# Kernel tuning notes

Hardware: AMD Instinct MI355X
Metric: run time of the kernel (lower is better)

The kernel has to match this reference:

```python
import jax, jax.numpy as jnp
import numpy as np

B, T, D, H, L = 1024, 512, 16, 30, 10


def setup_inputs() -> dict:
    key = jax.random.key(0)
    ks = jax.random.split(key, 8)
    s = 1.0 / np.sqrt(H)  # PyTorch RNN init scale (uniform +-1/sqrt(H)); normal*s is fine for a numeric baseline
    return {
        "x": jax.random.normal(ks[0], (B, T, D), dtype=jnp.float32),
        "W_ih0": jax.random.normal(ks[1], (H, D), dtype=jnp.float32) * s,
        "W_ih": jax.random.normal(ks[2], (L - 1, H, H), dtype=jnp.float32) * s,
        "W_hh": jax.random.normal(ks[3], (L, H, H), dtype=jnp.float32) * s,
        "b_ih": jax.random.normal(ks[4], (L, H), dtype=jnp.float32) * s,
        "b_hh": jax.random.normal(ks[5], (L, H), dtype=jnp.float32) * s,
        "fc_w": jax.random.normal(ks[6], (1, H), dtype=jnp.float32) * s,
        "fc_b": jax.random.normal(ks[7], (1,), dtype=jnp.float32) * s,
    }


def _rnn_layer(x, Wi, Wh, bi, bh):
    # x: [B, T, Din] -> [B, T, H]; h_t = tanh(x_t Wi^T + bi + h_{t-1} Wh^T + bh)
    xw = jnp.einsum("btd,hd->bth", x, Wi) + (bi + bh)  # fold both biases once
    h0 = jnp.zeros((x.shape[0], Wh.shape[0]), dtype=x.dtype)

    def step(h, xw_t):
        h = jnp.tanh(xw_t + h @ Wh.T)
        return h, h

    _, ys = jax.lax.scan(step, h0, jnp.swapaxes(xw, 0, 1))  # scan over time
    return jnp.swapaxes(ys, 0, 1)


def reference(x, W_ih0, W_ih, W_hh, b_ih, b_hh, fc_w, fc_b):
    out = _rnn_layer(x, W_ih0, W_hh[0], b_ih[0], b_hh[0])
    for l in range(1, L):
        out = _rnn_layer(out, W_ih[l - 1], W_hh[l], b_ih[l], b_hh[l])
    # fc on last timestep: [B, H] @ [H, 1] + b -> [B, 1]
    return out[:, -1, :] @ fc_w.T + fc_b
```

## Files before the change

kernel.cpp:

```cpp
#include <hip/hip_runtime.h>

#define TT 512
#define DD 16
#define HH 30
#define LL 10
#define C  4
#define TCH (TT / C)
#define RING 4
#define GRP 16
#define BLOCKT (LL * 64)
#define KPRE 2.885390081777927f

#define CC_H   512
#define SL_H   (C * CC_H)
#define LINK_H (RING * SL_H)

typedef _Float16 f16x8 __attribute__((ext_vector_type(8)));
typedef _Float16 h2    __attribute__((ext_vector_type(2)));
typedef float    f32x4 __attribute__((ext_vector_type(4)));

union U128 { uint4 u; f16x8 h; h2 p[4]; };

__device__ __forceinline__ float sigma_e(float d) {
    const float e = __builtin_amdgcn_exp2f(d);
    return __builtin_amdgcn_rcpf(e + 1.0f);
}

__device__ __forceinline__ int nu_of(int k) {
    return 16 * ((k >> 2) & 1) + 4 * (k >> 3) + (k & 3);
}

__device__ __forceinline__ void wait_ge(unsigned* f, unsigned tgt) {
    while (__hip_atomic_load(f, __ATOMIC_ACQUIRE,
                             __HIP_MEMORY_SCOPE_WORKGROUP) < tgt)
        __builtin_amdgcn_s_sleep(1);
}

__global__ __launch_bounds__(BLOCKT) void rnn_sig(
    const float* __restrict__ x,   const float* __restrict__ wi0,
    const float* __restrict__ wih, const float* __restrict__ whh,
    const float* __restrict__ bih, const float* __restrict__ bhh,
    const float* __restrict__ fcw, const float* __restrict__ fcb,
    float* __restrict__ out)
{
    extern __shared__ __align__(16) _Float16 link[];
    __shared__ unsigned flg[2 * LL];

    const int tid  = threadIdx.x;
    const int l    = tid >> 6;
    const int lane = tid & 63;
    const int n    = lane & 15;
    const int qq   = lane >> 4;
    const int b0   = blockIdx.x * GRP;

    f16x8 wain[2], waown[2];
    #pragma unroll
    for (int tile = 0; tile < 2; ++tile) {
        const int j = 16 * tile + n;
        #pragma unroll
        for (int i = 0; i < 8; ++i) {
            const int kap = 8 * qq + i;
            const int nu  = nu_of(kap);
            float vi = 0.f, vo = 0.f;
            if (j < HH) {
                if (l == 0) { if (kap < DD) vi =  wi0[j * DD + kap]; }
                else        { if (nu  < HH) vi = -2.f * wih[(l - 1) * 900 + j * HH + nu]; }
                if (nu < HH) vo = -2.f * whh[l * 900 + j * HH + nu];
            }
            wain[tile][i]  = (_Float16)(vi * KPRE);
            waown[tile][i] = (_Float16)(vo * KPRE);
        }
    }
    f32x4 cb[2];
    #pragma unroll
    for (int tile = 0; tile < 2; ++tile)
        #pragma unroll
        for (int r = 0; r < 4; ++r) {
            const int j2 = 16 * tile + 4 * qq + r;
            float v = 0.f;
            if (j2 < HH) {
                v = bih[l * HH + j2] + bhh[l * HH + j2];
                for (int k = 0; k < HH; ++k) v += whh[l * 900 + j2 * HH + k];
                if (l > 0)
                    for (int k = 0; k < HH; ++k) v += wih[(l - 1) * 900 + j2 * HH + k];
            }
            cb[tile][r] = v * KPRE;
        }
    float fcl[8];
    #pragma unroll
    for (int i = 0; i < 8; ++i) {
        const int nu = nu_of(8 * qq + i);
        fcl[i] = (nu < HH) ? -2.f * fcw[nu] : 0.f;
    }
    float fbv = fcb[0];
    for (int k = 0; k < HH; ++k) fbv += fcw[k];

    float4 xb[C][2];
    const float4* x4 = (const float4*)x;
    const size_t xbase = (size_t)(b0 + n) * TT * 4;
    if (l == 0 && qq < 2) {
        #pragma unroll
        for (int cc = 0; cc < C; ++cc) {
            xb[cc][0] = x4[xbase + cc * 4 + 2 * qq];
            xb[cc][1] = x4[xbase + cc * 4 + 2 * qq + 1];
        }
    }

    _Float16* lin_r = link + (l - 1) * LINK_H + lane * 8;
    _Float16* lin_w = link + l * LINK_H + lane * 8;

    f16x8 bown;
    #pragma unroll
    for (int i = 0; i < 8; ++i) bown[i] = (_Float16)0.5f;

    if (tid < 2 * LL) flg[tid] = 0u;
    __syncthreads();

    for (int pb = 0; pb < TCH; pb += RING) {
        #pragma unroll
        for (int sl = 0; sl < RING; ++sl) {
            const int pt = pb + sl;

            U128 binu[C];
            if (l == 0) {
                #pragma unroll
                for (int cc = 0; cc < C; ++cc) {
                    if (qq < 2) {
                        const float4 u = xb[cc][0], v = xb[cc][1];
                        binu[cc].p[0] = (h2)__builtin_amdgcn_cvt_pkrtz(u.x, u.y);
                        binu[cc].p[1] = (h2)__builtin_amdgcn_cvt_pkrtz(u.z, u.w);
                        binu[cc].p[2] = (h2)__builtin_amdgcn_cvt_pkrtz(v.x, v.y);
                        binu[cc].p[3] = (h2)__builtin_amdgcn_cvt_pkrtz(v.z, v.w);
                        if (pt + 1 < TCH) {
                            const int tn = (pt + 1) * C + cc;
                            xb[cc][0] = x4[xbase + tn * 4 + 2 * qq];
                            xb[cc][1] = x4[xbase + tn * 4 + 2 * qq + 1];
                        }
                    } else {
                        binu[cc].u = uint4{0u, 0u, 0u, 0u};
                    }
                }
            } else {
                wait_ge(&flg[l - 1], (unsigned)(pt + 1));
                #pragma unroll
                for (int cc = 0; cc < C; ++cc)
                    binu[cc].u = *(const uint4*)(lin_r + sl * SL_H + cc * CC_H);
            }

            f32x4 dp0[C], dp1[C];
            #pragma unroll
            for (int cc = 0; cc < C; ++cc) {
                dp0[cc] = __builtin_amdgcn_mfma_f32_16x16x32_f16(wain[0], binu[cc].h, cb[0], 0, 0, 0);
                dp1[cc] = __builtin_amdgcn_mfma_f32_16x16x32_f16(wain[1], binu[cc].h, cb[1], 0, 0, 0);
            }
            if (l > 0 && lane == 0)
                __hip_atomic_store(&flg[LL + l], (unsigned)(pt + 1),
                                   __ATOMIC_RELEASE, __HIP_MEMORY_SCOPE_WORKGROUP);
            if (l < LL - 1 && pt >= RING)
                wait_ge(&flg[LL + l + 1], (unsigned)(pt - RING + 1));

            #pragma unroll
            for (int cc = 0; cc < C; ++cc) {
                const f32x4 d0 = __builtin_amdgcn_mfma_f32_16x16x32_f16(waown[0], bown, dp0[cc], 0, 0, 0);
                const f32x4 d1 = __builtin_amdgcn_mfma_f32_16x16x32_f16(waown[1], bown, dp1[cc], 0, 0, 0);
                U128 uu;
                uu.p[0] = (h2)__builtin_amdgcn_cvt_pkrtz(sigma_e(d0[0]), sigma_e(d0[1]));
                uu.p[1] = (h2)__builtin_amdgcn_cvt_pkrtz(sigma_e(d0[2]), sigma_e(d0[3]));
                uu.p[2] = (h2)__builtin_amdgcn_cvt_pkrtz(sigma_e(d1[0]), sigma_e(d1[1]));
                uu.p[3] = (h2)__builtin_amdgcn_cvt_pkrtz(sigma_e(d1[2]), sigma_e(d1[3]));
                bown = uu.h;
                if (l < LL - 1)
                    *(uint4*)(lin_w + sl * SL_H + cc * CC_H) = uu.u;
            }
            if (l < LL - 1 && lane == 0)
                __hip_atomic_store(&flg[l], (unsigned)(pt + 1),
                                   __ATOMIC_RELEASE, __HIP_MEMORY_SCOPE_WORKGROUP);
        }
    }

    if (l == LL - 1) {
        float v = 0.f;
        #pragma unroll
        for (int i = 0; i < 8; ++i) v = fmaf((float)bown[i], fcl[i], v);
        v += __shfl_xor(v, 16);
        v += __shfl_xor(v, 32);
        if (qq == 0) out[b0 + n] = v + fbv;
    }
}

extern "C" void kernel_launch(void* const* d_in, const int* in_sizes, int n_in,
                              void* d_out, int out_size, void* d_ws, size_t ws_size,
                              hipStream_t stream) {
    const float* x   = (const float*)d_in[0];
    const float* wi0 = (const float*)d_in[1];
    const float* wih = (const float*)d_in[2];
    const float* whh = (const float*)d_in[3];
    const float* bih = (const float*)d_in[4];
    const float* bhh = (const float*)d_in[5];
    const float* fcw = (const float*)d_in[6];
    const float* fcb = (const float*)d_in[7];
    float* out = (float*)d_out;

    const size_t lds_bytes = (size_t)(LL - 1) * LINK_H * sizeof(_Float16);
    hipFuncSetAttribute((const void*)rnn_sig,
                        hipFuncAttributeMaxDynamicSharedMemorySize,
                        (int)lds_bytes);

    rnn_sig<<<1024 / GRP, BLOCKT, lds_bytes, stream>>>(x, wi0, wih, whh,
                                                       bih, bhh, fcw, fcb, out);
}
```

Baseline: 204.4 us.

## Double-buffer layer inputs and prefetch next slot before recurrent MFMA

Each layer wavefront now loads the next time slot's input from the LDS link (or converts prefetched x for layer 0) into a second register buffer while the current step's recurrent MFMAs and sigmoids run. This hides LDS read and flag-wait latency behind compute. The downstream back-pressure wait moves from every step to once per ring block, and the spin-wait drops s_sleep for lower wake latency. In exchange it uses more registers, and busy-polling with no sleep adds LDS traffic.

```diff
diff --git a/kernel.cpp b/kernel.cpp
--- a/kernel.cpp
+++ b/kernel.cpp
@@ -32,11 +32,10 @@
 
 __device__ __forceinline__ void wait_ge(unsigned* f, unsigned tgt) {
     while (__hip_atomic_load(f, __ATOMIC_ACQUIRE,
-                             __HIP_MEMORY_SCOPE_WORKGROUP) < tgt)
-        __builtin_amdgcn_s_sleep(1);
-}
-
-__global__ __launch_bounds__(BLOCKT) void rnn_sig(
+                             __HIP_MEMORY_SCOPE_WORKGROUP) < tgt) {}
+}
+
+__global__ __launch_bounds__(BLOCKT) void rnn_pipe(
     const float* __restrict__ x,   const float* __restrict__ wi0,
     const float* __restrict__ wih, const float* __restrict__ whh,
     const float* __restrict__ bih, const float* __restrict__ bhh,
@@ -95,69 +94,92 @@
     float fbv = fcb[0];
     for (int k = 0; k < HH; ++k) fbv += fcw[k];
 
+    _Float16* lin_r = link + (l - 1) * LINK_H + lane * 8;
+    _Float16* lin_w = link + l * LINK_H + lane * 8;
+
+    f16x8 bown;
+    #pragma unroll
+    for (int i = 0; i < 8; ++i) bown[i] = (_Float16)0.5f;
+
+    if (tid < 2 * LL) flg[tid] = 0u;
+    __syncthreads();
+
+    U128 bin[2][C];
     float4 xb[C][2];
     const float4* x4 = (const float4*)x;
     const size_t xbase = (size_t)(b0 + n) * TT * 4;
-    if (l == 0 && qq < 2) {
+
+    if (l == 0) {
         #pragma unroll
         for (int cc = 0; cc < C; ++cc) {
-            xb[cc][0] = x4[xbase + cc * 4 + 2 * qq];
-            xb[cc][1] = x4[xbase + cc * 4 + 2 * qq + 1];
-        }
-    }
-
-    _Float16* lin_r = link + (l - 1) * LINK_H + lane * 8;
-    _Float16* lin_w = link + l * LINK_H + lane * 8;
-
-    f16x8 bown;
-    #pragma unroll
-    for (int i = 0; i < 8; ++i) bown[i] = (_Float16)0.5f;
-
-    if (tid < 2 * LL) flg[tid] = 0u;
-    __syncthreads();
+            bin[0][cc].u = uint4{0u, 0u, 0u, 0u};
+            bin[1][cc].u = uint4{0u, 0u, 0u, 0u};
+        }
+        if (qq < 2) {
+            #pragma unroll
+            for (int cc = 0; cc < C; ++cc) {
+                const float4 u = x4[xbase + cc * 4 + 2 * qq];
+                const float4 v = x4[xbase + cc * 4 + 2 * qq + 1];
+                bin[0][cc].p[0] = (h2)__builtin_amdgcn_cvt_pkrtz(u.x, u.y);
+                bin[0][cc].p[1] = (h2)__builtin_amdgcn_cvt_pkrtz(u.z, u.w);
+                bin[0][cc].p[2] = (h2)__builtin_amdgcn_cvt_pkrtz(v.x, v.y);
+                bin[0][cc].p[3] = (h2)__builtin_amdgcn_cvt_pkrtz(v.z, v.w);
+                xb[cc][0] = x4[xbase + (C + cc) * 4 + 2 * qq];
+                xb[cc][1] = x4[xbase + (C + cc) * 4 + 2 * qq + 1];
+            }
+        }
+    } else {
+        wait_ge(&flg[l - 1], 1u);
+        #pragma unroll
+        for (int cc = 0; cc < C; ++cc)
+            bin[0][cc].u = *(const uint4*)(lin_r + cc * CC_H);
+    }
 
     for (int pb = 0; pb < TCH; pb += RING) {
+        if (l < LL - 1 && pb >= RING)
+            wait_ge(&flg[LL + l + 1], (unsigned)pb);
+
         #pragma unroll
         for (int sl = 0; sl < RING; ++sl) {
-            const int pt = pb + sl;
-
-            U128 binu[C];
-            if (l == 0) {
-                #pragma unroll
-                for (int cc = 0; cc < C; ++cc) {
-                    if (qq < 2) {
-                        const float4 u = xb[cc][0], v = xb[cc][1];
-                        binu[cc].p[0] = (h2)__builtin_amdgcn_cvt_pkrtz(u.x, u.y);
-                        binu[cc].p[1] = (h2)__builtin_amdgcn_cvt_pkrtz(u.z, u.w);
-                        binu[cc].p[2] = (h2)__builtin_amdgcn_cvt_pkrtz(v.x, v.y);
-                        binu[cc].p[3] = (h2)__builtin_amdgcn_cvt_pkrtz(v.z, v.w);
-                        if (pt + 1 < TCH) {
-                            const int tn = (pt + 1) * C + cc;
-                            xb[cc][0] = x4[xbase + tn * 4 + 2 * qq];
-                            xb[cc][1] = x4[xbase + tn * 4 + 2 * qq + 1];
-                        }
-                    } else {
-                        binu[cc].u = uint4{0u, 0u, 0u, 0u};
-                    }
-                }
-            } else {
-                wait_ge(&flg[l - 1], (unsigned)(pt + 1));
-                #pragma unroll
-                for (int cc = 0; cc < C; ++cc)
-                    binu[cc].u = *(const uint4*)(lin_r + sl * SL_H + cc * CC_H);
-            }
+            const int pt  = pb + sl;
+            const int cur = sl & 1;
+            const int nxt = cur ^ 1;
 
             f32x4 dp0[C], dp1[C];
             #pragma unroll
             for (int cc = 0; cc < C; ++cc) {
-                dp0[cc] = __builtin_amdgcn_mfma_f32_16x16x32_f16(wain[0], binu[cc].h, cb[0], 0, 0, 0);
-                dp1[cc] = __builtin_amdgcn_mfma_f32_16x16x32_f16(wain[1], binu[cc].h, cb[1], 0, 0, 0);
+                dp0[cc] = __builtin_amdgcn_mfma_f32_16x16x32_f16(wain[0], bin[cur][cc].h, cb[0], 0, 0, 0);
+                dp1[cc] = __builtin_amdgcn_mfma_f32_16x16x32_f16(wain[1], bin[cur][cc].h, cb[1], 0, 0, 0);
             }
             if (l > 0 && lane == 0)
                 __hip_atomic_store(&flg[LL + l], (unsigned)(pt + 1),
                                    __ATOMIC_RELEASE, __HIP_MEMORY_SCOPE_WORKGROUP);
-            if (l < LL - 1 && pt >= RING)
-                wait_ge(&flg[LL + l + 1], (unsigned)(pt - RING + 1));
+
+            if (pt + 1 < TCH) {
+                if (l == 0) {
+                    if (qq < 2) {
+                        #pragma unroll
+                        for (int cc = 0; cc < C; ++cc) {
+                            const float4 u = xb[cc][0], v = xb[cc][1];
+                            bin[nxt][cc].p[0] = (h2)__builtin_amdgcn_cvt_pkrtz(u.x, u.y);
+                            bin[nxt][cc].p[1] = (h2)__builtin_amdgcn_cvt_pkrtz(u.z, u.w);
+                            bin[nxt][cc].p[2] = (h2)__builtin_amdgcn_cvt_pkrtz(v.x, v.y);
+                            bin[nxt][cc].p[3] = (h2)__builtin_amdgcn_cvt_pkrtz(v.z, v.w);
+                            if (pt + 2 < TCH) {
+                                const int tn = (pt + 2) * C + cc;
+                                xb[cc][0] = x4[xbase + tn * 4 + 2 * qq];
+                                xb[cc][1] = x4[xbase + tn * 4 + 2 * qq + 1];
+                            }
+                        }
+                    }
+                } else {
+                    wait_ge(&flg[l - 1], (unsigned)(pt + 2));
+                    const int nsl = (sl + 1) & 3;
+                    #pragma unroll
+                    for (int cc = 0; cc < C; ++cc)
+                        bin[nxt][cc].u = *(const uint4*)(lin_r + nsl * SL_H + cc * CC_H);
+                }
+            }
 
             #pragma unroll
             for (int cc = 0; cc < C; ++cc) {
@@ -202,10 +224,10 @@
     float* out = (float*)d_out;
 
     const size_t lds_bytes = (size_t)(LL - 1) * LINK_H * sizeof(_Float16);
-    hipFuncSetAttribute((const void*)rnn_sig,
+    hipFuncSetAttribute((const void*)rnn_pipe,
                         hipFuncAttributeMaxDynamicSharedMemorySize,
                         (int)lds_bytes);
 
-    rnn_sig<<<1024 / GRP, BLOCKT, lds_bytes, stream>>>(x, wi0, wih, whh,
-                                                       bih, bhh, fcw, fcb, out);
-}
+    rnn_pipe<<<1024 / GRP, BLOCKT, lds_bytes, stream>>>(x, wi0, wih, whh,
+                                                        bih, bhh, fcw, fcb, out);
+}
```

Measured after the change: 235.3 us. +15.1%, slower.

## Interleave two batch groups per wave to hide recurrence latency

Applied to the files above, without the earlier changes.

Each block now processes two 16-row batch groups (A and B) per layer wave, interleaving their MFMA and sigmoid chains so that independent work fills the latency of the serial recurrence. The grid is halved and the LDS ring is shrunk from 4 to 2 slots so that total shared memory stays the same with doubled slot size. The wait on the downstream consumer flag is moved to the start of each step. The shallower ring may add stalls between layers, and the extra live registers could raise register pressure.

```diff
diff --git a/kernel.cpp b/kernel.cpp
--- a/kernel.cpp
+++ b/kernel.cpp
@@ -6,13 +6,15 @@
 #define LL 10
 #define C  4
 #define TCH (TT / C)
-#define RING 4
+#define RING 2
 #define GRP 16
+#define NG 2
 #define BLOCKT (LL * 64)
 #define KPRE 2.885390081777927f
 
 #define CC_H   512
-#define SL_H   (C * CC_H)
+#define SLG_H  (C * CC_H)
+#define SL_H   (NG * SLG_H)
 #define LINK_H (RING * SL_H)
 
 typedef _Float16 f16x8 __attribute__((ext_vector_type(8)));
@@ -36,7 +38,7 @@
         __builtin_amdgcn_s_sleep(1);
 }
 
-__global__ __launch_bounds__(BLOCKT) void rnn_sig(
+__global__ __launch_bounds__(BLOCKT) void rnn_dual2(
     const float* __restrict__ x,   const float* __restrict__ wi0,
     const float* __restrict__ wih, const float* __restrict__ whh,
     const float* __restrict__ bih, const float* __restrict__ bhh,
@@ -51,7 +53,7 @@
     const int lane = tid & 63;
     const int n    = lane & 15;
     const int qq   = lane >> 4;
-    const int b0   = blockIdx.x * GRP;
+    const int b0   = blockIdx.x * (GRP * NG);
 
     f16x8 wain[2], waown[2];
     #pragma unroll
@@ -95,82 +97,107 @@
     float fbv = fcb[0];
     for (int k = 0; k < HH; ++k) fbv += fcw[k];
 
-    float4 xb[C][2];
-    const float4* x4 = (const float4*)x;
-    const size_t xbase = (size_t)(b0 + n) * TT * 4;
-    if (l == 0 && qq < 2) {
-        #pragma unroll
-        for (int cc = 0; cc < C; ++cc) {
-            xb[cc][0] = x4[xbase + cc * 4 + 2 * qq];
-            xb[cc][1] = x4[xbase + cc * 4 + 2 * qq + 1];
-        }
-    }
-
     _Float16* lin_r = link + (l - 1) * LINK_H + lane * 8;
     _Float16* lin_w = link + l * LINK_H + lane * 8;
 
-    f16x8 bown;
-    #pragma unroll
-    for (int i = 0; i < 8; ++i) bown[i] = (_Float16)0.5f;
+    f16x8 bownA, bownB;
+    #pragma unroll
+    for (int i = 0; i < 8; ++i) { bownA[i] = (_Float16)0.5f; bownB[i] = (_Float16)0.5f; }
 
     if (tid < 2 * LL) flg[tid] = 0u;
     __syncthreads();
 
+    float4 xbA[C][2], xbB[C][2];
+    const float4* x4 = (const float4*)x;
+    const size_t xbA0 = (size_t)(b0 + n) * TT * 4;
+    const size_t xbB0 = (size_t)(b0 + GRP + n) * TT * 4;
+    if (l == 0 && qq < 2) {
+        #pragma unroll
+        for (int cc = 0; cc < C; ++cc) {
+            xbA[cc][0] = x4[xbA0 + cc * 4 + 2 * qq];
+            xbA[cc][1] = x4[xbA0 + cc * 4 + 2 * qq + 1];
+            xbB[cc][0] = x4[xbB0 + cc * 4 + 2 * qq];
+            xbB[cc][1] = x4[xbB0 + cc * 4 + 2 * qq + 1];
+        }
+    }
+
     for (int pb = 0; pb < TCH; pb += RING) {
         #pragma unroll
         for (int sl = 0; sl < RING; ++sl) {
             const int pt = pb + sl;
 
-            U128 binu[C];
+            if (l < LL - 1 && pt >= RING)
+                wait_ge(&flg[LL + l + 1], (unsigned)(pt - RING + 1));
+
+            U128 binA[C], binB[C];
             if (l == 0) {
                 #pragma unroll
                 for (int cc = 0; cc < C; ++cc) {
                     if (qq < 2) {
-                        const float4 u = xb[cc][0], v = xb[cc][1];
-                        binu[cc].p[0] = (h2)__builtin_amdgcn_cvt_pkrtz(u.x, u.y);
-                        binu[cc].p[1] = (h2)__builtin_amdgcn_cvt_pkrtz(u.z, u.w);
-                        binu[cc].p[2] = (h2)__builtin_amdgcn_cvt_pkrtz(v.x, v.y);
-                        binu[cc].p[3] = (h2)__builtin_amdgcn_cvt_pkrtz(v.z, v.w);
+                        float4 u = xbA[cc][0], v = xbA[cc][1];
+                        binA[cc].p[0] = (h2)__builtin_amdgcn_cvt_pkrtz(u.x, u.y);
+                        binA[cc].p[1] = (h2)__builtin_amdgcn_cvt_pkrtz(u.z, u.w);
+                        binA[cc].p[2] = (h2)__builtin_amdgcn_cvt_pkrtz(v.x, v.y);
+                        binA[cc].p[3] = (h2)__builtin_amdgcn_cvt_pkrtz(v.z, v.w);
+                        u = xbB[cc][0]; v = xbB[cc][1];
+                        binB[cc].p[0] = (h2)__builtin_amdgcn_cvt_pkrtz(u.x, u.y);
+                        binB[cc].p[1] = (h2)__builtin_amdgcn_cvt_pkrtz(u.z, u.w);
+                        binB[cc].p[2] = (h2)__builtin_amdgcn_cvt_pkrtz(v.x, v.y);
+                        binB[cc].p[3] = (h2)__builtin_amdgcn_cvt_pkrtz(v.z, v.w);
                         if (pt + 1 < TCH) {
                             const int tn = (pt + 1) * C + cc;
-                            xb[cc][0] = x4[xbase + tn * 4 + 2 * qq];
-                            xb[cc][1] = x4[xbase + tn * 4 + 2 * qq + 1];
+                            xbA[cc][0] = x4[xbA0 + tn * 4 + 2 * qq];
+                            xbA[cc][1] = x4[xbA0 + tn * 4 + 2 * qq + 1];
+                            xbB[cc][0] = x4[xbB0 + tn * 4 + 2 * qq];
+                            xbB[cc][1] = x4[xbB0 + tn * 4 + 2 * qq + 1];
                         }
                     } else {
-                        binu[cc].u = uint4{0u, 0u, 0u, 0u};
+                        binA[cc].u = uint4{0u, 0u, 0u, 0u};
+                        binB[cc].u = uint4{0u, 0u, 0u, 0u};
                     }
                 }
             } else {
                 wait_ge(&flg[l - 1], (unsigned)(pt + 1));
                 #pragma unroll
-                for (int cc = 0; cc < C; ++cc)
-                    binu[cc].u = *(const uint4*)(lin_r + sl * SL_H + cc * CC_H);
-            }
-
-            f32x4 dp0[C], dp1[C];
+                for (int cc = 0; cc < C; ++cc) {
+                    binA[cc].u = *(const uint4*)(lin_r + (sl * NG + 0) * SLG_H + cc * CC_H);
+                    binB[cc].u = *(const uint4*)(lin_r + (sl * NG + 1) * SLG_H + cc * CC_H);
+                }
+            }
+
+            f32x4 dpA0[C], dpA1[C], dpB0[C], dpB1[C];
             #pragma unroll
             for (int cc = 0; cc < C; ++cc) {
-                dp0[cc] = __builtin_amdgcn_mfma_f32_16x16x32_f16(wain[0], binu[cc].h, cb[0], 0, 0, 0);
-                dp1[cc] = __builtin_amdgcn_mfma_f32_16x16x32_f16(wain[1], binu[cc].h, cb[1], 0, 0, 0);
+                dpA0[cc] = __builtin_amdgcn_mfma_f32_16x16x32_f16(wain[0], binA[cc].h, cb[0], 0, 0, 0);
+                dpB0[cc] = __builtin_amdgcn_mfma_f32_16x16x32_f16(wain[0], binB[cc].h, cb[0], 0, 0, 0);
+                dpA1[cc] = __builtin_amdgcn_mfma_f32_16x16x32_f16(wain[1], binA[cc].h, cb[1], 0, 0, 0);
+                dpB1[cc] = __builtin_amdgcn_mfma_f32_16x16x32_f16(wain[1], binB[cc].h, cb[1], 0, 0, 0);
             }
             if (l > 0 && lane == 0)
                 __hip_atomic_store(&flg[LL + l], (unsigned)(pt + 1),
                                    __ATOMIC_RELEASE, __HIP_MEMORY_SCOPE_WORKGROUP);
-            if (l < LL - 1 && pt >= RING)
-                wait_ge(&flg[LL + l + 1], (unsigned)(pt - RING + 1));
 
             #pragma unroll
             for (int cc = 0; cc < C; ++cc) {
-                const f32x4 d0 = __builtin_amdgcn_mfma_f32_16x16x32_f16(waown[0], bown, dp0[cc], 0, 0, 0);
-                const f32x4 d1 = __builtin_amdgcn_mfma_f32_16x16x32_f16(waown[1], bown, dp1[cc], 0, 0, 0);
-                U128 uu;
-                uu.p[0] = (h2)__builtin_amdgcn_cvt_pkrtz(sigma_e(d0[0]), sigma_e(d0[1]));
-                uu.p[1] = (h2)__builtin_amdgcn_cvt_pkrtz(sigma_e(d0[2]), sigma_e(d0[3]));
-                uu.p[2] = (h2)__builtin_amdgcn_cvt_pkrtz(sigma_e(d1[0]), sigma_e(d1[1]));
-                uu.p[3] = (h2)__builtin_amdgcn_cvt_pkrtz(sigma_e(d1[2]), sigma_e(d1[3]));
-                bown = uu.h;
-                if (l < LL - 1)
-                    *(uint4*)(lin_w + sl * SL_H + cc * CC_H) = uu.u;
+                const f32x4 dA0 = __builtin_amdgcn_mfma_f32_16x16x32_f16(waown[0], bownA, dpA0[cc], 0, 0, 0);
+                const f32x4 dB0 = __builtin_amdgcn_mfma_f32_16x16x32_f16(waown[0], bownB, dpB0[cc], 0, 0, 0);
+                const f32x4 dA1 = __builtin_amdgcn_mfma_f32_16x16x32_f16(waown[1], bownA, dpA1[cc], 0, 0, 0);
+                const f32x4 dB1 = __builtin_amdgcn_mfma_f32_16x16x32_f16(waown[1], bownB, dpB1[cc], 0, 0, 0);
+                U128 uA, uB;
+                uA.p[0] = (h2)__builtin_amdgcn_cvt_pkrtz(sigma_e(dA0[0]), sigma_e(dA0[1]));
+                uB.p[0] = (h2)__builtin_amdgcn_cvt_pkrtz(sigma_e(dB0[0]), sigma_e(dB0[1]));
+                uA.p[1] = (h2)__builtin_amdgcn_cvt_pkrtz(sigma_e(dA0[2]), sigma_e(dA0[3]));
+                uB.p[1] = (h2)__builtin_amdgcn_cvt_pkrtz(sigma_e(dB0[2]), sigma_e(dB0[3]));
+                uA.p[2] = (h2)__builtin_amdgcn_cvt_pkrtz(sigma_e(dA1[0]), sigma_e(dA1[1]));
+                uB.p[2] = (h2)__builtin_amdgcn_cvt_pkrtz(sigma_e(dB1[0]), sigma_e(dB1[1]));
+                uA.p[3] = (h2)__builtin_amdgcn_cvt_pkrtz(sigma_e(dA1[2]), sigma_e(dA1[3]));
+                uB.p[3] = (h2)__builtin_amdgcn_cvt_pkrtz(sigma_e(dB1[2]), sigma_e(dB1[3]));
+                bownA = uA.h;
+                bownB = uB.h;
+                if (l < LL - 1) {
+                    *(uint4*)(lin_w + (sl * NG + 0) * SLG_H + cc * CC_H) = uA.u;
+                    *(uint4*)(lin_w + (sl * NG + 1) * SLG_H + cc * CC_H) = uB.u;
+                }
             }
             if (l < LL - 1 && lane == 0)
                 __hip_atomic_store(&flg[l], (unsigned)(pt + 1),
@@ -179,12 +206,18 @@
     }
 
     if (l == LL - 1) {
-        float v = 0.f;
-        #pragma unroll
-        for (int i = 0; i < 8; ++i) v = fmaf((float)bown[i], fcl[i], v);
-        v += __shfl_xor(v, 16);
-        v += __shfl_xor(v, 32);
-        if (qq == 0) out[b0 + n] = v + fbv;
+        float vA = 0.f, vB = 0.f;
+        #pragma unroll
+        for (int i = 0; i < 8; ++i) {
+            vA = fmaf((float)bownA[i], fcl[i], vA);
+            vB = fmaf((float)bownB[i], fcl[i], vB);
+        }
+        vA += __shfl_xor(vA, 16);  vB += __shfl_xor(vB, 16);
+        vA += __shfl_xor(vA, 32);  vB += __shfl_xor(vB, 32);
+        if (qq == 0) {
+            out[b0 + n]       = vA + fbv;
+            out[b0 + GRP + n] = vB + fbv;
+        }
     }
 }
 
@@ -202,10 +235,10 @@
     float* out = (float*)d_out;
 
     const size_t lds_bytes = (size_t)(LL - 1) * LINK_H * sizeof(_Float16);
-    hipFuncSetAttribute((const void*)rnn_sig,
+    hipFuncSetAttribute((const void*)rnn_dual2,
                         hipFuncAttributeMaxDynamicSharedMemorySize,
                         (int)lds_bytes);
 
-    rnn_sig<<<1024 / GRP, BLOCKT, lds_bytes, stream>>>(x, wi0, wih, whh,
-                                                       bih, bhh, fcw, fcb, out);
-}
+    rnn_dual2<<<1024 / (GRP * NG), BLOCKT, lds_bytes, stream>>>(
+        x, wi0, wih, whh, bih, bhh, fcw, fcb, out);
+}
```

Measured after the change: 439.0 us. 2.15x slower.

## Double the wavefront pipeline chunk to eight steps with half-chunk processing and lighter flag publishes

Applied to the files above, without the earlier changes.

Each layer wavefront now handles 8 timesteps per handoff instead of 4, processed as two halves of 4, with a ring depth of 2 instead of 4 (same LDS size). The aim is to halve the number of inter-layer flag waits and publishes. The release-ordered atomic stores are replaced by an explicit lgkmcnt wait plus a relaxed store, and the wait on the downstream consumer now comes before the input wait. The cost is a longer pipeline fill/drain across the 10 layers and coarser-grained overlap between neighbouring layers.

```diff
diff --git a/kernel.cpp b/kernel.cpp
--- a/kernel.cpp
+++ b/kernel.cpp
@@ -4,15 +4,17 @@
 #define DD 16
 #define HH 30
 #define LL 10
-#define C  4
-#define TCH (TT / C)
-#define RING 4
+#define CHK 8
+#define HC  4
+#define NCH (TT / CHK)
+#define RING 2
 #define GRP 16
 #define BLOCKT (LL * 64)
 #define KPRE 2.885390081777927f
 
 #define CC_H   512
-#define SL_H   (C * CC_H)
+#define HALF_H (HC * CC_H)
+#define SL_H   (CHK * CC_H)
 #define LINK_H (RING * SL_H)
 
 typedef _Float16 f16x8 __attribute__((ext_vector_type(8)));
@@ -36,7 +38,13 @@
         __builtin_amdgcn_s_sleep(1);
 }
 
-__global__ __launch_bounds__(BLOCKT) void rnn_sig(
+__device__ __forceinline__ void publish(unsigned* f, unsigned v) {
+    __builtin_amdgcn_sched_barrier(0);
+    asm volatile("s_waitcnt lgkmcnt(0)" ::: "memory");
+    __hip_atomic_store(f, v, __ATOMIC_RELAXED, __HIP_MEMORY_SCOPE_WORKGROUP);
+}
+
+__global__ __launch_bounds__(BLOCKT) void rnn_c8(
     const float* __restrict__ x,   const float* __restrict__ wi0,
     const float* __restrict__ wih, const float* __restrict__ whh,
     const float* __restrict__ bih, const float* __restrict__ bhh,
@@ -95,12 +103,12 @@
     float fbv = fcb[0];
     for (int k = 0; k < HH; ++k) fbv += fcw[k];
 
-    float4 xb[C][2];
+    float4 xb[HC][2];
     const float4* x4 = (const float4*)x;
     const size_t xbase = (size_t)(b0 + n) * TT * 4;
     if (l == 0 && qq < 2) {
         #pragma unroll
-        for (int cc = 0; cc < C; ++cc) {
+        for (int cc = 0; cc < HC; ++cc) {
             xb[cc][0] = x4[xbase + cc * 4 + 2 * qq];
             xb[cc][1] = x4[xbase + cc * 4 + 2 * qq + 1];
         }
@@ -116,65 +124,70 @@
     if (tid < 2 * LL) flg[tid] = 0u;
     __syncthreads();
 
-    for (int pb = 0; pb < TCH; pb += RING) {
+    for (int pb = 0; pb < NCH; pb += RING) {
         #pragma unroll
         for (int sl = 0; sl < RING; ++sl) {
             const int pt = pb + sl;
 
-            U128 binu[C];
-            if (l == 0) {
-                #pragma unroll
-                for (int cc = 0; cc < C; ++cc) {
-                    if (qq < 2) {
-                        const float4 u = xb[cc][0], v = xb[cc][1];
-                        binu[cc].p[0] = (h2)__builtin_amdgcn_cvt_pkrtz(u.x, u.y);
-                        binu[cc].p[1] = (h2)__builtin_amdgcn_cvt_pkrtz(u.z, u.w);
-                        binu[cc].p[2] = (h2)__builtin_amdgcn_cvt_pkrtz(v.x, v.y);
-                        binu[cc].p[3] = (h2)__builtin_amdgcn_cvt_pkrtz(v.z, v.w);
-                        if (pt + 1 < TCH) {
-                            const int tn = (pt + 1) * C + cc;
-                            xb[cc][0] = x4[xbase + tn * 4 + 2 * qq];
-                            xb[cc][1] = x4[xbase + tn * 4 + 2 * qq + 1];
-                        }
-                    } else {
-                        binu[cc].u = uint4{0u, 0u, 0u, 0u};
-                    }
-                }
-            } else {
-                wait_ge(&flg[l - 1], (unsigned)(pt + 1));
-                #pragma unroll
-                for (int cc = 0; cc < C; ++cc)
-                    binu[cc].u = *(const uint4*)(lin_r + sl * SL_H + cc * CC_H);
-            }
-
-            f32x4 dp0[C], dp1[C];
-            #pragma unroll
-            for (int cc = 0; cc < C; ++cc) {
-                dp0[cc] = __builtin_amdgcn_mfma_f32_16x16x32_f16(wain[0], binu[cc].h, cb[0], 0, 0, 0);
-                dp1[cc] = __builtin_amdgcn_mfma_f32_16x16x32_f16(wain[1], binu[cc].h, cb[1], 0, 0, 0);
-            }
-            if (l > 0 && lane == 0)
-                __hip_atomic_store(&flg[LL + l], (unsigned)(pt + 1),
-                                   __ATOMIC_RELEASE, __HIP_MEMORY_SCOPE_WORKGROUP);
             if (l < LL - 1 && pt >= RING)
                 wait_ge(&flg[LL + l + 1], (unsigned)(pt - RING + 1));
+            if (l > 0)
+                wait_ge(&flg[l - 1], (unsigned)(pt + 1));
 
             #pragma unroll
-            for (int cc = 0; cc < C; ++cc) {
-                const f32x4 d0 = __builtin_amdgcn_mfma_f32_16x16x32_f16(waown[0], bown, dp0[cc], 0, 0, 0);
-                const f32x4 d1 = __builtin_amdgcn_mfma_f32_16x16x32_f16(waown[1], bown, dp1[cc], 0, 0, 0);
-                U128 uu;
-                uu.p[0] = (h2)__builtin_amdgcn_cvt_pkrtz(sigma_e(d0[0]), sigma_e(d0[1]));
-                uu.p[1] = (h2)__builtin_amdgcn_cvt_pkrtz(sigma_e(d0[2]), sigma_e(d0[3]));
-                uu.p[2] = (h2)__builtin_amdgcn_cvt_pkrtz(sigma_e(d1[0]), sigma_e(d1[1]));
-                uu.p[3] = (h2)__builtin_amdgcn_cvt_pkrtz(sigma_e(d1[2]), sigma_e(d1[3]));
-                bown = uu.h;
-                if (l < LL - 1)
-                    *(uint4*)(lin_w + sl * SL_H + cc * CC_H) = uu.u;
+            for (int h = 0; h < 2; ++h) {
+                U128 binu[HC];
+                if (l == 0) {
+                    #pragma unroll
+                    for (int cc = 0; cc < HC; ++cc) {
+                        if (qq < 2) {
+                            const float4 u = xb[cc][0], v = xb[cc][1];
+                            binu[cc].p[0] = (h2)__builtin_amdgcn_cvt_pkrtz(u.x, u.y);
+                            binu[cc].p[1] = (h2)__builtin_amdgcn_cvt_pkrtz(u.z, u.w);
+                            binu[cc].p[2] = (h2)__builtin_amdgcn_cvt_pkrtz(v.x, v.y);
+                            binu[cc].p[3] = (h2)__builtin_amdgcn_cvt_pkrtz(v.z, v.w);
+                            const int gh = pt * 2 + h + 1;
+                            if (gh < TT / HC) {
+                                const int tn = gh * HC + cc;
+                                xb[cc][0] = x4[xbase + tn * 4 + 2 * qq];
+                                xb[cc][1] = x4[xbase + tn * 4 + 2 * qq + 1];
+                            }
+                        } else {
+                            binu[cc].u = uint4{0u, 0u, 0u, 0u};
+                        }
+                    }
+                } else {
+                    #pragma unroll
+                    for (int cc = 0; cc < HC; ++cc)
+                        binu[cc].u = *(const uint4*)(lin_r + sl * SL_H + h * HALF_H
+                                                     + cc * CC_H);
+                }
+
+                f32x4 dp0[HC], dp1[HC];
+                #pragma unroll
+                for (int cc = 0; cc < HC; ++cc) {
+                    dp0[cc] = __builtin_amdgcn_mfma_f32_16x16x32_f16(wain[0], binu[cc].h, cb[0], 0, 0, 0);
+                    dp1[cc] = __builtin_amdgcn_mfma_f32_16x16x32_f16(wain[1], binu[cc].h, cb[1], 0, 0, 0);
+                }
+                if (h == 1 && l > 0 && lane == 0)
+                    publish(&flg[LL + l], (unsigned)(pt + 1));
+
+                #pragma unroll
+                for (int cc = 0; cc < HC; ++cc) {
+                    const f32x4 d0 = __builtin_amdgcn_mfma_f32_16x16x32_f16(waown[0], bown, dp0[cc], 0, 0, 0);
+                    const f32x4 d1 = __builtin_amdgcn_mfma_f32_16x16x32_f16(waown[1], bown, dp1[cc], 0, 0, 0);
+                    U128 uu;
+                    uu.p[0] = (h2)__builtin_amdgcn_cvt_pkrtz(sigma_e(d0[0]), sigma_e(d0[1]));
+                    uu.p[1] = (h2)__builtin_amdgcn_cvt_pkrtz(sigma_e(d0[2]), sigma_e(d0[3]));
+                    uu.p[2] = (h2)__builtin_amdgcn_cvt_pkrtz(sigma_e(d1[0]), sigma_e(d1[1]));
+                    uu.p[3] = (h2)__builtin_amdgcn_cvt_pkrtz(sigma_e(d1[2]), sigma_e(d1[3]));
+                    bown = uu.h;
+                    if (l < LL - 1)
+                        *(uint4*)(lin_w + sl * SL_H + h * HALF_H + cc * CC_H) = uu.u;
+                }
             }
             if (l < LL - 1 && lane == 0)
-                __hip_atomic_store(&flg[l], (unsigned)(pt + 1),
-                                   __ATOMIC_RELEASE, __HIP_MEMORY_SCOPE_WORKGROUP);
+                publish(&flg[l], (unsigned)(pt + 1));
         }
     }
 
@@ -202,10 +215,10 @@
     float* out = (float*)d_out;
 
     const size_t lds_bytes = (size_t)(LL - 1) * LINK_H * sizeof(_Float16);
-    hipFuncSetAttribute((const void*)rnn_sig,
+    hipFuncSetAttribute((const void*)rnn_c8,
                         hipFuncAttributeMaxDynamicSharedMemorySize,
                         (int)lds_bytes);
 
-    rnn_sig<<<1024 / GRP, BLOCKT, lds_bytes, stream>>>(x, wi0, wih, whh,
-                                                       bih, bhh, fcw, fcb, out);
-}
+    rnn_c8<<<1024 / GRP, BLOCKT, lds_bytes, stream>>>(x, wi0, wih, whh,
+                                                      bih, bhh, fcw, fcb, out);
+}
```

Result: no change. 201.8 us (median of 2 runs) (-1.3%).
